# Performance work log

Hardware: AMD Instinct MI355X
Metric: run time of the kernel (lower is better)

The kernel has to match this reference:

```python
import jax, jax.numpy as jnp
import numpy as np

NUM_HEADS = 8
TOP_K = 2
ROUTER_EPS = 1e-5
LN_EPS = 1e-5
ROPE_BASE = 10000.0


def _layernorm(x, g, b):
    m = x.mean(-1, keepdims=True)
    v = ((x - m) ** 2).mean(-1, keepdims=True)
    return (x - m) * jax.lax.rsqrt(v + LN_EPS) * g + b


def _rope_tables(frames, height, width, head_dim, dtype):
    # dim split per axis; head_dim divisible by 3 with even parts (96 -> 32/32/32)
    dpa = head_dim // 3

    def freqs(n, d):
        inv = 1.0 / (ROPE_BASE ** (jnp.arange(0, d, 2, dtype=jnp.float32) / d))
        f = jnp.outer(jnp.arange(n, dtype=jnp.float32), inv)
        return jnp.concatenate([f, f], axis=-1)  # [n, d]

    fx, fy, ft = freqs(width, dpa), freqs(height, dpa), freqs(frames, dpa)

    def grid(ax, ay, at):
        gx = jnp.broadcast_to(ax[None, None, :, :], (frames, height, width, dpa))
        gy = jnp.broadcast_to(ay[None, :, None, :], (frames, height, width, dpa))
        gt = jnp.broadcast_to(at[:, None, None, :], (frames, height, width, dpa))
        return jnp.concatenate([gx, gy, gt], -1).reshape(frames * height * width, 3 * dpa)

    cos = grid(jnp.cos(fx), jnp.cos(fy), jnp.cos(ft)).astype(dtype)
    sin = grid(jnp.sin(fx), jnp.sin(fy), jnp.sin(ft)).astype(dtype)
    return cos, sin


def _apply_rope(x, cos, sin):
    # x: [B, H, S, hd]; cos/sin: [S, hd] (broadcast over B, H)
    h = x.shape[-1] // 2
    rot = jnp.concatenate([-x[..., h:], x[..., :h]], axis=-1)
    return x * cos + rot * sin


def _expert(x, g, u, d):
    # SwiGLU expert: down(silu(gate(x)) * up(x))
    return (jax.nn.silu(x @ g) * (x @ u)) @ d


def _block(x, cos, sin, ln1_g, ln1_b, w_qkv, w_out, gate_w,
           eg, eu, ed, sg, su, sd, ln2_g, ln2_b):
    B, S, D = x.shape
    hd = D // NUM_HEADS
    # --- 3D-RoPE attention (pre-LN, non-causal) ---
    xn = _layernorm(x, ln1_g, ln1_b)
    qkv = (xn @ w_qkv).reshape(B, S, 3, NUM_HEADS, hd)
    q = jnp.moveaxis(qkv[:, :, 0], 1, 2)  # [B, H, S, hd]
    k = jnp.moveaxis(qkv[:, :, 1], 1, 2)
    v = jnp.moveaxis(qkv[:, :, 2], 1, 2)
    q = _apply_rope(q, cos, sin)
    k = _apply_rope(k, cos, sin)
    scores = jnp.einsum('bhqd,bhkd->bhqk', q, k) * (hd ** -0.5)
    attn = jax.nn.softmax(scores, axis=-1)
    o = jnp.einsum('bhqk,bhkd->bhqd', attn, v)
    o = jnp.moveaxis(o, 1, 2).reshape(B, S, D) @ w_out
    x = x + o
    # --- temporal MoE (top-k routing + shared expert) ---
    xf = x.reshape(-1, D)
    probs = jax.nn.softmax(xf @ gate_w, axis=-1)
    topv, topi = jax.lax.top_k(probs, TOP_K)
    topv = topv / (topv.sum(-1, keepdims=True) + ROUTER_EPS)
    E = eg.shape[0]
    # combine weight per (token, expert): sum over k slots routed to that expert
    comb = jnp.sum(topv[..., None] * (topi[..., None] == jnp.arange(E)), axis=1)  # [N, E]
    out = _expert(xf, sg, su, sd)  # shared expert on all tokens
    for e in range(E):
        out = out + comb[:, e:e + 1] * _expert(xf, eg[e], eu[e], ed[e])
    return _layernorm(x + out.reshape(B, S, D), ln2_g, ln2_b)


def setup_inputs() -> dict:
    key = jax.random.key(0)
    ks = jax.random.split(key, 10)
    B, S, D, F, E, L = 2, 2048, 768, 3072, 4, 2
    s = 0.02
    return {
        'x': jax.random.normal(ks[0], (B, S, D), jnp.float32),
        'height': 16, 'width': 16, 'frames': 8,
        'ln1_g': jnp.ones((L, D), jnp.float32),
        'ln1_b': jnp.zeros((L, D), jnp.float32),
        'w_qkv': jax.random.normal(ks[1], (L, D, 3 * D), jnp.float32) * s,
        'w_out': jax.random.normal(ks[2], (L, D, D), jnp.float32) * s,
        'gate_w': jax.random.normal(ks[3], (L, D, E), jnp.float32) * 0.01,
        'eg': jax.random.normal(ks[4], (L, E, D, F), jnp.float32) * s,
        'eu': jax.random.normal(ks[5], (L, E, D, F), jnp.float32) * s,
        'ed': jax.random.normal(ks[6], (L, E, F, D), jnp.float32) * s,
        'sg': jax.random.normal(ks[7], (L, D, F), jnp.float32) * s,
        'su': jax.random.normal(ks[8], (L, D, F), jnp.float32) * s,
        'sd': jax.random.normal(ks[9], (L, F, D), jnp.float32) * s,
        'ln2_g': jnp.ones((L, D), jnp.float32),
        'ln2_b': jnp.zeros((L, D), jnp.float32),
    }


def reference(x, height, width, frames, ln1_g, ln1_b, w_qkv, w_out, gate_w,
              eg, eu, ed, sg, su, sd, ln2_g, ln2_b):
    hd = x.shape[-1] // NUM_HEADS
    cos, sin = _rope_tables(frames, height, width, hd, x.dtype)
    for i in range(ln1_g.shape[0]):
        x = _block(x, cos, sin, ln1_g[i], ln1_b[i], w_qkv[i], w_out[i], gate_w[i],
                   eg[i], eu[i], ed[i], sg[i], su[i], sd[i], ln2_g[i], ln2_b[i])
    return x
```

## Files before the change

### kernel.cpp

```cpp
#include <hip/hip_runtime.h>
#include <stdint.h>

#define S_LEN 2048
#define DM    768
#define NHEAD 8
#define HDIM  96
#define HDP   128
#define FF    3072
#define FF2   6144
#define NEXP  4
#define NTOK  4096
#define NBH   16
#define HBROWS (2 * NTOK)

typedef unsigned short u16;
typedef short bf16x8 __attribute__((ext_vector_type(8)));
typedef float f32x4 __attribute__((ext_vector_type(4)));
typedef __attribute__((address_space(1))) void* gptr_t;
typedef __attribute__((address_space(3))) void* lptr_t;

__device__ __forceinline__ u16 f2bf(float f) {
  union { float f; uint32_t u; } v; v.f = f;
  uint32_t r = v.u + 0x7FFFu + ((v.u >> 16) & 1u);
  return (u16)(r >> 16);
}
__device__ __forceinline__ float bf2f(u16 h) {
  union { uint32_t u; float f; } v; v.u = ((uint32_t)h) << 16;
  return v.f;
}
__device__ __forceinline__ void split2(float f, u16& hi, u16& lo) {
  u16 h = f2bf(f);
  lo = f2bf(f - bf2f(h));
  hi = h;
}
__device__ __forceinline__ float siluf(float g) {
  return g / (1.0f + expf(-g));
}
__device__ __forceinline__ void gload16(const void* g, void* l) {
  __builtin_amdgcn_global_load_lds((gptr_t)(void*)g, (lptr_t)l, 16, 0, 0);
}
__device__ __forceinline__ int swz(int byte) {
  return byte ^ (((byte >> 7) & 3) << 4);
}

template<int MODE>
__global__ __launch_bounds__(256) void gemm_nt(
    const u16* __restrict__ A, const u16* __restrict__ B, void* __restrict__ Cv,
    int M, int N, int K, int lda, int ldb, long sA, long sB, long sC, int kspl,
    u16* __restrict__ hb)
{
  __shared__ u16 As[2][128 * 32];
  __shared__ u16 Bs[2][128 * 32];
  const int z = blockIdx.z;
  const int bh = z / kspl;
  const int kc = z - bh * kspl;
  const u16* Az = A + (long)bh * sA;
  const u16* Bz = B + (long)bh * sB;
  const int brow = blockIdx.y << 7;
  const int bcol = blockIdx.x << 7;
  const int tid = threadIdx.x;
  const int wid = tid >> 6;
  const int lane = tid & 63;
  const int wr = (wid >> 1) << 6;
  const int wc = (wid & 1) << 6;

  f32x4 acc[4][4] = {};
  const int a0 = (wid << 11) + (lane << 4);

  auto stage = [&](int buf, int k0) {
#pragma unroll
    for (int c = 0; c < 2; ++c) {
      int ab = a0 + (c << 10);
      int lb = swz(ab);
      int row = ab >> 6;
      int kcol = (lb & 63) >> 1;
      int ld = (wid << 11) + (c << 10);
      gload16(Az + (long)(brow + row) * lda + (k0 + kcol), (char*)As[buf] + ld);
      gload16(Bz + (long)(bcol + row) * ldb + (k0 + kcol), (char*)Bs[buf] + ld);
    }
  };

  const int kt = K / kspl;
  const int kbeg = kc * kt;
  const int nt = kt >> 5;
  stage(0, kbeg);
  __syncthreads();
  for (int t = 0; t < nt; ++t) {
    const int cur = t & 1;
    if (t + 1 < nt) stage(cur ^ 1, kbeg + ((t + 1) << 5));
    bf16x8 af[4], bfr[4];
    const int lr = lane & 15;
    const int lk = (lane >> 4) << 4;
#pragma unroll
    for (int m = 0; m < 4; ++m)
      af[m] = *(const bf16x8*)((const char*)As[cur] + swz((((wr + m * 16 + lr) << 6) + lk)));
#pragma unroll
    for (int n = 0; n < 4; ++n)
      bfr[n] = *(const bf16x8*)((const char*)Bs[cur] + swz((((wc + n * 16 + lr) << 6) + lk)));
#pragma unroll
    for (int m = 0; m < 4; ++m)
#pragma unroll
      for (int n = 0; n < 4; ++n)
        acc[m][n] = __builtin_amdgcn_mfma_f32_16x16x32_bf16(af[m], bfr[n], acc[m][n], 0, 0, 0);
    if (t + 1 < nt) __syncthreads();
  }

  const int crow0 = brow + wr + ((lane >> 4) << 2);
  const int ccol0 = bcol + wc + (lane & 15);
  const long cbase = (long)bh * sC;
  if constexpr (MODE == 5) {
    const int pbase = (bcol + wc) >> 5;
#pragma unroll
    for (int m = 0; m < 4; ++m)
#pragma unroll
      for (int np = 0; np < 2; ++np)
#pragma unroll
        for (int j = 0; j < 4; ++j) {
          int r = crow0 + m * 16 + j;
          float g = acc[m][2 * np][j], u = acc[m][2 * np + 1][j];
          int hcol = ((pbase + np) << 4) + (lane & 15);
          hb[(long)r * FF + hcol] = f2bf(siluf(g) * u);
        }
  } else {
#pragma unroll
    for (int m = 0; m < 4; ++m)
#pragma unroll
      for (int n = 0; n < 4; ++n)
#pragma unroll
        for (int j = 0; j < 4; ++j) {
          long idx = cbase + (long)(crow0 + m * 16 + j) * N + (ccol0 + n * 16);
          float v = acc[m][n][j];
          if constexpr (MODE == 2) ((u16*)Cv)[idx] = f2bf(v);
          else if constexpr (MODE == 3) unsafeAtomicAdd((float*)Cv + idx, v);
          else ((float*)Cv)[idx] = v;
        }
  }
}

template<int MODE>
__global__ __launch_bounds__(256) void gemm3_nt(
    const u16* __restrict__ Ah, const u16* __restrict__ Al,
    const u16* __restrict__ Bh, const u16* __restrict__ Bl,
    float* __restrict__ C,
    int M, int N, int K, int lda, int ldb, long sA, long sB, long sC, int kspl,
    u16* __restrict__ hbh, u16* __restrict__ hbl)
{
  __shared__ u16 Ash[2][128 * 32], Asl[2][128 * 32];
  __shared__ u16 Bsh[2][128 * 32], Bsl[2][128 * 32];
  const int z = blockIdx.z;
  const int bh = z / kspl;
  const int kc = z - bh * kspl;
  const u16* Azh = Ah + (long)bh * sA;
  const u16* Azl = Al + (long)bh * sA;
  const u16* Bzh = Bh + (long)bh * sB;
  const u16* Bzl = Bl + (long)bh * sB;
  const int brow = blockIdx.y << 7;
  const int bcol = blockIdx.x << 7;
  const int tid = threadIdx.x;
  const int wid = tid >> 6;
  const int lane = tid & 63;
  const int wr = (wid >> 1) << 6;
  const int wc = (wid & 1) << 6;

  f32x4 acc[4][4] = {};
  const int a0 = (wid << 11) + (lane << 4);

  auto stage = [&](int buf, int k0) {
#pragma unroll
    for (int c = 0; c < 2; ++c) {
      int ab = a0 + (c << 10);
      int lb = swz(ab);
      int row = ab >> 6;
      int kcol = (lb & 63) >> 1;
      long ao = (long)(brow + row) * lda + (k0 + kcol);
      long bo = (long)(bcol + row) * ldb + (k0 + kcol);
      int ld = (wid << 11) + (c << 10);
      gload16(Azh + ao, (char*)Ash[buf] + ld);
      gload16(Azl + ao, (char*)Asl[buf] + ld);
      gload16(Bzh + bo, (char*)Bsh[buf] + ld);
      gload16(Bzl + bo, (char*)Bsl[buf] + ld);
    }
  };

  const int kt = K / kspl;
  const int kbeg = kc * kt;
  const int nt = kt >> 5;
  stage(0, kbeg);
  __syncthreads();
  for (int t = 0; t < nt; ++t) {
    const int cur = t & 1;
    if (t + 1 < nt) stage(cur ^ 1, kbeg + ((t + 1) << 5));
    const int lr = lane & 15;
    const int lk = (lane >> 4) << 4;
    bf16x8 ah[4], al[4], bh_[4], bl[4];
#pragma unroll
    for (int m = 0; m < 4; ++m) {
      int off = swz(((wr + m * 16 + lr) << 6) + lk);
      ah[m] = *(const bf16x8*)((const char*)Ash[cur] + off);
      al[m] = *(const bf16x8*)((const char*)Asl[cur] + off);
    }
#pragma unroll
    for (int n = 0; n < 4; ++n) {
      int off = swz(((wc + n * 16 + lr) << 6) + lk);
      bh_[n] = *(const bf16x8*)((const char*)Bsh[cur] + off);
      bl[n] = *(const bf16x8*)((const char*)Bsl[cur] + off);
    }
#pragma unroll
    for (int m = 0; m < 4; ++m)
#pragma unroll
      for (int n = 0; n < 4; ++n) {
        acc[m][n] = __builtin_amdgcn_mfma_f32_16x16x32_bf16(al[m], bh_[n], acc[m][n], 0, 0, 0);
        acc[m][n] = __builtin_amdgcn_mfma_f32_16x16x32_bf16(ah[m], bl[n], acc[m][n], 0, 0, 0);
        acc[m][n] = __builtin_amdgcn_mfma_f32_16x16x32_bf16(ah[m], bh_[n], acc[m][n], 0, 0, 0);
      }
    if (t + 1 < nt) __syncthreads();
  }

  const int crow0 = brow + wr + ((lane >> 4) << 2);
  const int ccol0 = bcol + wc + (lane & 15);
  const long cbase = (long)bh * sC;
  if constexpr (MODE == 5) {
    const int pbase = (bcol + wc) >> 5;
#pragma unroll
    for (int m = 0; m < 4; ++m)
#pragma unroll
      for (int np = 0; np < 2; ++np)
#pragma unroll
        for (int j = 0; j < 4; ++j) {
          int r = crow0 + m * 16 + j;
          float g = acc[m][2 * np][j], u = acc[m][2 * np + 1][j];
          float h = siluf(g) * u;
          int hcol = ((pbase + np) << 4) + (lane & 15);
          u16 hh, ll; split2(h, hh, ll);
          hbh[(long)r * FF + hcol] = hh;
          hbl[(long)r * FF + hcol] = ll;
        }
  } else {
#pragma unroll
    for (int m = 0; m < 4; ++m)
#pragma unroll
      for (int n = 0; n < 4; ++n)
#pragma unroll
        for (int j = 0; j < 4; ++j) {
          long idx = cbase + (long)(crow0 + m * 16 + j) * N + (ccol0 + n * 16);
          if constexpr (MODE == 3) unsafeAtomicAdd(&C[idx], acc[m][n][j]);
          else C[idx] = acc[m][n][j];
        }
  }
}

template<int MODE>
__global__ __launch_bounds__(256) void gemm3i_nt(
    const u16* __restrict__ Ah, const u16* __restrict__ Al,
    const u16* __restrict__ Bh, const u16* __restrict__ Bl,
    float* __restrict__ C, int N, int K, int lda, int ldb, int ldc,
    const int* __restrict__ perm, const int* __restrict__ cnt,
    const int* __restrict__ cbase, int kspl, long wstride,
    u16* __restrict__ hbh, u16* __restrict__ hbl, const float* __restrict__ comb)
{
  const int z = blockIdx.z;
  const int e = z / kspl;
  const int kc = z - e * kspl;
  const int cn = cnt[e];
  const int brow = blockIdx.y << 7;
  if (brow >= cn) return;
  const int cb = cbase[e];
  const int* pe = perm + e * NTOK;
  const u16* Bhe = Bh + (long)e * wstride;
  const u16* Ble = Bl + (long)e * wstride;
  __shared__ u16 Ash[2][128 * 32], Asl[2][128 * 32];
  __shared__ u16 Bsh[2][128 * 32], Bsl[2][128 * 32];
  const int bcol = blockIdx.x << 7;
  const int tid = threadIdx.x;
  const int wid = tid >> 6;
  const int lane = tid & 63;
  const int wr = (wid >> 1) << 6;
  const int wc = (wid & 1) << 6;

  f32x4 acc[4][4] = {};
  const int a0 = (wid << 11) + (lane << 4);

  int arow[2];
#pragma unroll
  for (int c = 0; c < 2; ++c) {
    int ab = a0 + (c << 10);
    int row = ab >> 6;
    int g = brow + row;
    if constexpr (MODE == 5) {
      arow[c] = (g < cn) ? pe[g] : pe[brow];
    } else {
      arow[c] = cb + ((g < cn) ? g : (cn - 1));
    }
  }

  auto stage = [&](int buf, int k0) {
#pragma unroll
    for (int c = 0; c < 2; ++c) {
      int ab = a0 + (c << 10);
      int lb = swz(ab);
      int row = ab >> 6;
      int kcol = (lb & 63) >> 1;
      int ld = (wid << 11) + (c << 10);
      gload16(Ah + (long)arow[c] * lda + (k0 + kcol), (char*)Ash[buf] + ld);
      gload16(Al + (long)arow[c] * lda + (k0 + kcol), (char*)Asl[buf] + ld);
      long bo = (long)(bcol + row) * ldb + (k0 + kcol);
      gload16(Bhe + bo, (char*)Bsh[buf] + ld);
      gload16(Ble + bo, (char*)Bsl[buf] + ld);
    }
  };

  const int kt = K / kspl;
  const int kbeg = kc * kt;
  const int nt = kt >> 5;
  stage(0, kbeg);
  __syncthreads();
  for (int t = 0; t < nt; ++t) {
    const int cur = t & 1;
    if (t + 1 < nt) stage(cur ^ 1, kbeg + ((t + 1) << 5));
    const int lr = lane & 15;
    const int lk = (lane >> 4) << 4;
    bf16x8 ah[4], al[4], bh_[4], bl[4];
#pragma unroll
    for (int m = 0; m < 4; ++m) {
      int off = swz(((wr + m * 16 + lr) << 6) + lk);
      ah[m] = *(const bf16x8*)((const char*)Ash[cur] + off);
      al[m] = *(const bf16x8*)((const char*)Asl[cur] + off);
    }
#pragma unroll
    for (int n = 0; n < 4; ++n) {
      int off = swz(((wc + n * 16 + lr) << 6) + lk);
      bh_[n] = *(const bf16x8*)((const char*)Bsh[cur] + off);
      bl[n] = *(const bf16x8*)((const char*)Bsl[cur] + off);
    }
#pragma unroll
    for (int m = 0; m < 4; ++m)
#pragma unroll
      for (int n = 0; n < 4; ++n) {
        acc[m][n] = __builtin_amdgcn_mfma_f32_16x16x32_bf16(al[m], bh_[n], acc[m][n], 0, 0, 0);
        acc[m][n] = __builtin_amdgcn_mfma_f32_16x16x32_bf16(ah[m], bl[n], acc[m][n], 0, 0, 0);
        acc[m][n] = __builtin_amdgcn_mfma_f32_16x16x32_bf16(ah[m], bh_[n], acc[m][n], 0, 0, 0);
      }
    if (t + 1 < nt) __syncthreads();
  }

  const int crow0 = brow + wr + ((lane >> 4) << 2);
  const int ccol0 = bcol + wc + (lane & 15);
  if constexpr (MODE == 5) {
    const int pbase = (bcol + wc) >> 5;
#pragma unroll
    for (int m = 0; m < 4; ++m)
#pragma unroll
      for (int j = 0; j < 4; ++j) {
        int r = crow0 + m * 16 + j;
        if (r < cn) {
          float w = comb[pe[r] * 4 + e];
#pragma unroll
          for (int np = 0; np < 2; ++np) {
            float g = acc[m][2 * np][j], u = acc[m][2 * np + 1][j];
            float h = siluf(g) * u * w;
            int hcol = ((pbase + np) << 4) + (lane & 15);
            u16 hh, ll; split2(h, hh, ll);
            hbh[(long)(cb + r) * FF + hcol] = hh;
            hbl[(long)(cb + r) * FF + hcol] = ll;
          }
        }
      }
  } else {
#pragma unroll
    for (int m = 0; m < 4; ++m)
#pragma unroll
      for (int n = 0; n < 4; ++n)
#pragma unroll
        for (int j = 0; j < 4; ++j) {
          int r = crow0 + m * 16 + j;
          if (r < cn) {
            int col = ccol0 + n * 16;
            unsafeAtomicAdd(&C[(long)pe[r] * ldc + col], acc[m][n][j]);
          }
        }
  }
}

template<int MODE>
__global__ __launch_bounds__(256) void gemmi_nt(
    const u16* __restrict__ A, const u16* __restrict__ B, void* __restrict__ Cv,
    int N, int K, int lda, int ldb, int ldc,
    const int* __restrict__ perm, const int* __restrict__ cnt,
    const int* __restrict__ cbase, int kspl, long wstride,
    u16* __restrict__ hb, const float* __restrict__ comb)
{
  const int z = blockIdx.z;
  const int e = z / kspl;
  const int kc = z - e * kspl;
  const int cn = cnt[e];
  const int brow = blockIdx.y << 7;
  if (brow >= cn) return;
  const int cb = cbase[e];
  const int* pe = perm + e * NTOK;
  const u16* Be = B + (long)e * wstride;
  __shared__ u16 As[2][128 * 32];
  __shared__ u16 Bs[2][128 * 32];
  const int bcol = blockIdx.x << 7;
  const int tid = threadIdx.x;
  const int wid = tid >> 6;
  const int lane = tid & 63;
  const int wr = (wid >> 1) << 6;
  const int wc = (wid & 1) << 6;

  f32x4 acc[4][4] = {};
  const int a0 = (wid << 11) + (lane << 4);

  int arow[2];
#pragma unroll
  for (int c = 0; c < 2; ++c) {
    int ab = a0 + (c << 10);
    int row = ab >> 6;
    int g = brow + row;
    if constexpr (MODE == 5) {
      arow[c] = (g < cn) ? pe[g] : pe[brow];
    } else {
      arow[c] = cb + ((g < cn) ? g : (cn - 1));
    }
  }

  auto stage = [&](int buf, int k0) {
#pragma unroll
    for (int c = 0; c < 2; ++c) {
      int ab = a0 + (c << 10);
      int lb = swz(ab);
      int row = ab >> 6;
      int kcol = (lb & 63) >> 1;
      int ld = (wid << 11) + (c << 10);
      gload16(A + (long)arow[c] * lda + (k0 + kcol), (char*)As[buf] + ld);
      gload16(Be + (long)(bcol + row) * ldb + (k0 + kcol), (char*)Bs[buf] + ld);
    }
  };

  const int kt = K / kspl;
  const int kbeg = kc * kt;
  const int nt = kt >> 5;
  stage(0, kbeg);
  __syncthreads();
  for (int t = 0; t < nt; ++t) {
    const int cur = t & 1;
    if (t + 1 < nt) stage(cur ^ 1, kbeg + ((t + 1) << 5));
    bf16x8 af[4], bfr[4];
    const int lr = lane & 15;
    const int lk = (lane >> 4) << 4;
#pragma unroll
    for (int m = 0; m < 4; ++m)
      af[m] = *(const bf16x8*)((const char*)As[cur] + swz((((wr + m * 16 + lr) << 6) + lk)));
#pragma unroll
    for (int n = 0; n < 4; ++n)
      bfr[n] = *(const bf16x8*)((const char*)Bs[cur] + swz((((wc + n * 16 + lr) << 6) + lk)));
#pragma unroll
    for (int m = 0; m < 4; ++m)
#pragma unroll
      for (int n = 0; n < 4; ++n)
        acc[m][n] = __builtin_amdgcn_mfma_f32_16x16x32_bf16(af[m], bfr[n], acc[m][n], 0, 0, 0);
    if (t + 1 < nt) __syncthreads();
  }

  const int crow0 = brow + wr + ((lane >> 4) << 2);
  const int ccol0 = bcol + wc + (lane & 15);
  if constexpr (MODE == 5) {
    const int pbase = (bcol + wc) >> 5;
#pragma unroll
    for (int m = 0; m < 4; ++m)
#pragma unroll
      for (int j = 0; j < 4; ++j) {
        int r = crow0 + m * 16 + j;
        if (r < cn) {
          float w = comb[pe[r] * 4 + e];
#pragma unroll
          for (int np = 0; np < 2; ++np) {
            float g = acc[m][2 * np][j], u = acc[m][2 * np + 1][j];
            int hcol = ((pbase + np) << 4) + (lane & 15);
            hb[(long)(cb + r) * FF + hcol] = f2bf(siluf(g) * u * w);
          }
        }
      }
  } else {
#pragma unroll
    for (int m = 0; m < 4; ++m)
#pragma unroll
      for (int n = 0; n < 4; ++n)
#pragma unroll
        for (int j = 0; j < 4; ++j) {
          int r = crow0 + m * 16 + j;
          if (r < cn) {
            int col = ccol0 + n * 16;
            unsafeAtomicAdd((float*)Cv + (long)pe[r] * ldc + col, acc[m][n][j]);
          }
        }
  }
}

__global__ __launch_bounds__(256, 2) void fattn_k(
    const u16* __restrict__ qh, const u16* __restrict__ ql,
    const u16* __restrict__ kh, const u16* __restrict__ kl,
    const u16* __restrict__ vth, const u16* __restrict__ vtl,
    u16* __restrict__ omh, u16* __restrict__ oml, float scale)
{
  __shared__ u16 Ksh[64 * 128], Ksl[64 * 128];
  __shared__ u16 Vsh[128 * 64], Vsl[128 * 64];
  const int bh = blockIdx.x;
  const int qt = blockIdx.y;
  const int tid = threadIdx.x, wid = tid >> 6, lane = tid & 63;
  const int lr = lane & 15, lg = lane >> 4;
  const int q0 = qt * 64 + wid * 16;
  const long bhoff = (long)bh * S_LEN * HDP;
  const u16* Qh = qh + bhoff;  const u16* Ql = ql + bhoff;
  const u16* Kgh = kh + bhoff; const u16* Kgl = kl + bhoff;
  const u16* Vgh = vth + bhoff; const u16* Vgl = vtl + bhoff;

  bf16x8 qfh[4], qfl[4];
#pragma unroll
  for (int kk = 0; kk < 4; ++kk) {
    long o = (long)(q0 + lr) * HDP + kk * 32 + lg * 8;
    qfh[kk] = *(const bf16x8*)(Qh + o);
    qfl[kk] = *(const bf16x8*)(Ql + o);
  }

  f32x4 oacc[6] = {};
  float rm[4], rls[4];
#pragma unroll
  for (int j = 0; j < 4; ++j) { rm[j] = -1e30f; rls[j] = 0.f; }

  for (int t = 0; t < S_LEN / 64; ++t) {
    __syncthreads();
#pragma unroll
    for (int c = 0; c < 4; ++c) {
      int off = (tid + (c << 8)) << 4;
      {
        int lb = off ^ ((((off >> 8) & 7)) << 4);
        int row = lb >> 8, colh = (lb & 255) >> 1;
        long src = (long)(t * 64 + row) * HDP + colh;
        gload16(Kgh + src, (char*)Ksh + off);
        gload16(Kgl + src, (char*)Ksl + off);
      }
      {
        int lb = off ^ ((((off >> 7) & 7)) << 4);
        int row = lb >> 7, colh = (lb & 127) >> 1;
        long src = (long)row * S_LEN + t * 64 + colh;
        gload16(Vgh + src, (char*)Vsh + off);
        gload16(Vgl + src, (char*)Vsl + off);
      }
    }
    __syncthreads();

    f32x4 sacc[4] = {};
#pragma unroll
    for (int kk = 0; kk < 4; ++kk) {
      bf16x8 kbh[4], kbl[4];
#pragma unroll
      for (int n = 0; n < 4; ++n) {
        int byte = ((n * 16 + lr) << 8) + (kk << 6) + (lg << 4);
        byte ^= ((byte >> 8) & 7) << 4;
        kbh[n] = *(const bf16x8*)((const char*)Ksh + byte);
        kbl[n] = *(const bf16x8*)((const char*)Ksl + byte);
      }
      __builtin_amdgcn_s_setprio(1);
#pragma unroll
      for (int n = 0; n < 4; ++n) {
        sacc[n] = __builtin_amdgcn_mfma_f32_16x16x32_bf16(qfl[kk], kbh[n], sacc[n], 0, 0, 0);
        sacc[n] = __builtin_amdgcn_mfma_f32_16x16x32_bf16(qfh[kk], kbl[n], sacc[n], 0, 0, 0);
        sacc[n] = __builtin_amdgcn_mfma_f32_16x16x32_bf16(qfh[kk], kbh[n], sacc[n], 0, 0, 0);
      }
      __builtin_amdgcn_s_setprio(0);
    }
    __syncthreads();

#pragma unroll
    for (int j = 0; j < 4; ++j) {
      float mx = fmaxf(fmaxf(sacc[0][j], sacc[1][j]),
                       fmaxf(sacc[2][j], sacc[3][j])) * scale;
      mx = fmaxf(mx, __shfl_xor(mx, 1));
      mx = fmaxf(mx, __shfl_xor(mx, 2));
      mx = fmaxf(mx, __shfl_xor(mx, 4));
      mx = fmaxf(mx, __shfl_xor(mx, 8));
      float mnew = fmaxf(rm[j], mx);
      float corr = __expf(rm[j] - mnew);
      rm[j] = mnew;
      float ps = 0.f;
#pragma unroll
      for (int n = 0; n < 4; ++n) {
        float p = __expf(sacc[n][j] * scale - mnew);
        sacc[n][j] = p; ps += p;
      }
      ps += __shfl_xor(ps, 1); ps += __shfl_xor(ps, 2);
      ps += __shfl_xor(ps, 4); ps += __shfl_xor(ps, 8);
      rls[j] = rls[j] * corr + ps;
#pragma unroll
      for (int n2 = 0; n2 < 6; ++n2) oacc[n2][j] *= corr;
    }

    char* Pwh = (char*)Ksh + (wid << 11);
    char* Pwl = (char*)Ksl + (wid << 11);
#pragma unroll
    for (int n = 0; n < 4; ++n)
#pragma unroll
      for (int j = 0; j < 4; ++j) {
        int row = lg * 4 + j;
        int byte = (row << 7) + ((n * 16 + lr) << 1);
        byte ^= ((byte >> 7) & 7) << 4;
        u16 h, l; split2(sacc[n][j], h, l);
        *(u16*)(Pwh + byte) = h;
        *(u16*)(Pwl + byte) = l;
      }
    bf16x8 pah[2], pal[2];
#pragma unroll
    for (int kk = 0; kk < 2; ++kk) {
      int byte = (lr << 7) + (kk << 6) + (lg << 4);
      byte ^= ((byte >> 7) & 7) << 4;
      pah[kk] = *(const bf16x8*)(Pwh + byte);
      pal[kk] = *(const bf16x8*)(Pwl + byte);
    }

#pragma unroll
    for (int kk = 0; kk < 2; ++kk) {
      bf16x8 vbh[6], vbl[6];
#pragma unroll
      for (int n2 = 0; n2 < 6; ++n2) {
        int byte = ((n2 * 16 + lr) << 7) + (kk << 6) + (lg << 4);
        byte ^= ((byte >> 7) & 7) << 4;
        vbh[n2] = *(const bf16x8*)((const char*)Vsh + byte);
        vbl[n2] = *(const bf16x8*)((const char*)Vsl + byte);
      }
      __builtin_amdgcn_s_setprio(1);
#pragma unroll
      for (int n2 = 0; n2 < 6; ++n2) {
        oacc[n2] = __builtin_amdgcn_mfma_f32_16x16x32_bf16(pal[kk], vbh[n2], oacc[n2], 0, 0, 0);
        oacc[n2] = __builtin_amdgcn_mfma_f32_16x16x32_bf16(pah[kk], vbl[n2], oacc[n2], 0, 0, 0);
        oacc[n2] = __builtin_amdgcn_mfma_f32_16x16x32_bf16(pah[kk], vbh[n2], oacc[n2], 0, 0, 0);
      }
      __builtin_amdgcn_s_setprio(0);
    }
  }

  const int b = bh >> 3, h = bh & 7;
#pragma unroll
  for (int j = 0; j < 4; ++j) {
    float inv = 1.0f / rls[j];
    int q = q0 + lg * 4 + j;
    long base = ((long)(b * S_LEN + q)) * DM + h * HDIM;
#pragma unroll
    for (int n2 = 0; n2 < 6; ++n2) {
      int d = n2 * 16 + lr;
      u16 hh, ll; split2(oacc[n2][j] * inv, hh, ll);
      omh[base + d] = hh; oml[base + d] = ll;
    }
  }
}

__global__ void wconv_t(const float* __restrict__ in, u16* __restrict__ outh,
                        u16* __restrict__ outl, int R, int C, int ilv,
                        long inStride, long outStride) {
  __shared__ float tile[32][33];
  long z = blockIdx.z;
  in += z * inStride; outh += z * outStride;
  if (outl) outl += z * outStride;
  int c0 = blockIdx.x << 5, r0 = blockIdx.y << 5;
  int tx = threadIdx.x;
  for (int rr = threadIdx.y; rr < 32; rr += 8)
    tile[rr][tx] = in[(long)(r0 + rr) * C + (c0 + tx)];
  __syncthreads();
  for (int rr = threadIdx.y; rr < 32; rr += 8) {
    u16 h, l; split2(tile[tx][rr], h, l);
    int f = c0 + rr;
    long orow = (ilv < 0) ? f : (((f >> 4) << 5) + (ilv << 4) + (f & 15));
    long o = orow * R + (r0 + tx);
    outh[o] = h;
    if (outl) outl[o] = l;
  }
}

__global__ __launch_bounds__(256) void ln_k(const float* __restrict__ in,
    const float* __restrict__ g, const float* __restrict__ b,
    float* __restrict__ outf, u16* __restrict__ outh, u16* __restrict__ outl) {
  int row = blockIdx.x;
  const float* x = in + (long)row * DM;
  int tid = threadIdx.x;
  float v[3], s = 0.f, ss = 0.f;
#pragma unroll
  for (int i = 0; i < 3; ++i) { v[i] = x[tid + (i << 8)]; s += v[i]; ss += v[i] * v[i]; }
  __shared__ float red[2][4];
  for (int o = 32; o; o >>= 1) { s += __shfl_down(s, o); ss += __shfl_down(ss, o); }
  int wid = tid >> 6, lane = tid & 63;
  if (!lane) { red[0][wid] = s; red[1][wid] = ss; }
  __syncthreads();
  s = red[0][0] + red[0][1] + red[0][2] + red[0][3];
  ss = red[1][0] + red[1][1] + red[1][2] + red[1][3];
  float mean = s * (1.f / DM);
  float var = ss * (1.f / DM) - mean * mean;
  float rs = rsqrtf(var + 1e-5f);
#pragma unroll
  for (int i = 0; i < 3; ++i) {
    int c = tid + (i << 8);
    float y = (v[i] - mean) * rs * g[c] + b[c];
    if (outf) outf[(long)row * DM + c] = y;
    if (outh) { u16 h, l; split2(y, h, l); outh[(long)row * DM + c] = h; outl[(long)row * DM + c] = l; }
  }
}

__global__ void rope_tables_k(float* __restrict__ cosT, float* __restrict__ sinT) {
  int s = blockIdx.x, d = threadIdx.x;
  int xc = s & 15, y = (s >> 4) & 15, t = s >> 8;
  int axis = d / 32, fi = d & 15;
  int coord = axis == 0 ? xc : (axis == 1 ? y : t);
  float inv = powf(10000.0f, -(float)fi / 16.0f);
  float ang = (float)coord * inv;
  cosT[s * HDIM + d] = cosf(ang);
  sinT[s * HDIM + d] = sinf(ang);
}

__global__ __launch_bounds__(256) void rope_apply_k(const float* __restrict__ qkv,
    const float* __restrict__ cosT, const float* __restrict__ sinT,
    u16* __restrict__ qh, u16* __restrict__ ql,
    u16* __restrict__ kh, u16* __restrict__ kl) {
  int bs = blockIdx.x;
  int b = bs >> 11, s = bs & 2047;
  const float* base = qkv + ((long)(b * S_LEN + s) * 3) * DM;
  for (int idx = threadIdx.x; idx < DM; idx += 256) {
    int h = idx / HDIM, d = idx - h * HDIM;
    float c = cosT[s * HDIM + d], sn = sinT[s * HDIM + d];
    int pair = (d < 48) ? idx + 48 : idx - 48;
    float qv = base[idx], kv = base[DM + idx];
    float qr = (d < 48) ? -base[pair] : base[pair];
    float kr = (d < 48) ? -base[DM + pair] : base[DM + pair];
    long o = ((long)(b * NHEAD + h) * S_LEN + s) * HDP + d;
    u16 hh, ll;
    split2(qv * c + qr * sn, hh, ll); qh[o] = hh; ql[o] = ll;
    split2(kv * c + kr * sn, hh, ll); kh[o] = hh; kl[o] = ll;
  }
  int t = threadIdx.x;
  int h = t >> 5, d = HDIM + (t & 31);
  long o = ((long)(b * NHEAD + h) * S_LEN + s) * HDP + d;
  qh[o] = 0; ql[o] = 0; kh[o] = 0; kl[o] = 0;
}

__global__ void v_transpose_k(const float* __restrict__ qkv,
                              u16* __restrict__ vh, u16* __restrict__ vl) {
  __shared__ float tile[32][33];
  int bh = blockIdx.z, b = bh >> 3, h = bh & 7;
  int s0 = blockIdx.x << 5, d0 = blockIdx.y << 5;
  int tx = threadIdx.x;
  for (int r = threadIdx.y; r < 32; r += 8) {
    int s = s0 + r, d = d0 + tx;
    float v = 0.f;
    if (d < HDIM) v = qkv[((long)(b * S_LEN + s) * 3 + 2) * DM + h * HDIM + d];
    tile[r][tx] = v;
  }
  __syncthreads();
  for (int r = threadIdx.y; r < 32; r += 8) {
    int d = d0 + r;
    u16 hh, ll; split2(tile[tx][r], hh, ll);
    long o = ((long)bh * HDP + d) * S_LEN + (s0 + tx);
    vh[o] = hh; vl[o] = ll;
  }
}

__global__ __launch_bounds__(256) void router_k(const float* __restrict__ x,
    const float* __restrict__ gw, float* __restrict__ comb, int* __restrict__ mask) {
  int tok = blockIdx.x * 4 + (threadIdx.x >> 6);
  int lane = threadIdx.x & 63;
  const float* xr = x + (long)tok * DM;
  float a0 = 0, a1 = 0, a2 = 0, a3 = 0;
  for (int i = lane; i < DM; i += 64) {
    float xv = xr[i];
    const float* g = gw + i * 4;
    a0 += xv * g[0]; a1 += xv * g[1]; a2 += xv * g[2]; a3 += xv * g[3];
  }
  for (int o = 32; o; o >>= 1) {
    a0 += __shfl_down(a0, o); a1 += __shfl_down(a1, o);
    a2 += __shfl_down(a2, o); a3 += __shfl_down(a3, o);
  }
  if (lane == 0) {
    float p[4] = {a0, a1, a2, a3};
    float mx = fmaxf(fmaxf(p[0], p[1]), fmaxf(p[2], p[3]));
    float s = 0.f;
    for (int e = 0; e < 4; ++e) { p[e] = expf(p[e] - mx); s += p[e]; }
    for (int e = 0; e < 4; ++e) p[e] /= s;
    int i1 = 0;
    for (int e = 1; e < 4; ++e) if (p[e] > p[i1]) i1 = e;
    int i2 = -1;
    for (int e = 0; e < 4; ++e) if (e != i1 && (i2 < 0 || p[e] > p[i2])) i2 = e;
    float ssum = p[i1] + p[i2] + 1e-5f;
    float out[4] = {0, 0, 0, 0};
    out[i1] = p[i1] / ssum; out[i2] = p[i2] / ssum;
    for (int e = 0; e < 4; ++e) comb[tok * 4 + e] = out[e];
    mask[tok] = (1 << i1) | (1 << i2);
  }
}

__global__ void scan_k(const int* __restrict__ mask, int* __restrict__ perm,
                       int* __restrict__ cnt) {
  __shared__ int sd[256];
  __shared__ int base;
  int tid = threadIdx.x;
  int e = blockIdx.x;
  if (tid == 0) base = 0;
  __syncthreads();
  for (int c = 0; c < NTOK / 256; ++c) {
    int tok = c * 256 + tid;
    int f = (mask[tok] >> e) & 1;
    sd[tid] = f;
    __syncthreads();
    for (int s = 1; s < 256; s <<= 1) {
      int v = (tid >= s) ? sd[tid - s] : 0;
      __syncthreads();
      sd[tid] += v;
      __syncthreads();
    }
    if (f) perm[e * NTOK + base + sd[tid] - 1] = tok;
    int tot = sd[255];
    __syncthreads();
    if (tid == 0) base += tot;
    __syncthreads();
  }
  if (tid == 0) cnt[e] = base;
}

__global__ void cbase_k(const int* __restrict__ cnt, int* __restrict__ cbase) {
  if (threadIdx.x == 0) {
    int b = 0;
    for (int e = 0; e < NEXP; ++e) { cbase[e] = b; b += cnt[e]; }
  }
}

__global__ void f2b_k(const float* __restrict__ src, u16* __restrict__ dst, long n) {
  long i = (long)blockIdx.x * 256 + threadIdx.x;
  if (i < n) dst[i] = f2bf(src[i]);
}

__global__ void f2bsplit_k(const float* __restrict__ src, u16* __restrict__ dh,
                           u16* __restrict__ dl, long n) {
  long i = (long)blockIdx.x * 256 + threadIdx.x;
  if (i < n) { u16 h, l; split2(src[i], h, l); dh[i] = h; dl[i] = l; }
}

extern "C" void kernel_launch(void* const* d_in, const int* in_sizes, int n_in,
                              void* d_out, int out_size, void* d_ws, size_t ws_size,
                              hipStream_t stream) {
  (void)in_sizes; (void)n_in; (void)out_size; (void)ws_size;
  const float* x_in  = (const float*)d_in[0];
  const float* ln1_g = (const float*)d_in[4];
  const float* ln1_b = (const float*)d_in[5];
  const float* w_qkv = (const float*)d_in[6];
  const float* w_out = (const float*)d_in[7];
  const float* gatew = (const float*)d_in[8];
  const float* eg    = (const float*)d_in[9];
  const float* eu    = (const float*)d_in[10];
  const float* ed    = (const float*)d_in[11];
  const float* sg    = (const float*)d_in[12];
  const float* su    = (const float*)d_in[13];
  const float* sd    = (const float*)d_in[14];
  const float* ln2_g = (const float*)d_in[15];
  const float* ln2_b = (const float*)d_in[16];

  float* xc = (float*)d_out;
  char* W = (char*)d_ws;
  size_t off = 0;
  auto alloc = [&](size_t bytes) {
    size_t o = off; off = (off + bytes + 255) & ~(size_t)255; return o;
  };
  size_t o_cos  = alloc((size_t)S_LEN * HDIM * 4);
  size_t o_sin  = alloc((size_t)S_LEN * HDIM * 4);
  size_t o_xnh  = alloc((size_t)NTOK * DM * 2);
  size_t o_xnl  = alloc((size_t)NTOK * DM * 2);
  size_t o_comb = alloc((size_t)NTOK * 4 * 4);
  size_t o_mask = alloc((size_t)NTOK * 4);
  size_t o_perm = alloc((size_t)NEXP * NTOK * 4);
  size_t o_cnt  = alloc(256);
  size_t o_cb   = alloc(256);
  const size_t EGU_B = (size_t)NEXP * FF2 * DM * 2;
  const size_t SGU_B = (size_t)FF2 * DM * 2;
  const size_t SD_B  = (size_t)DM * FF * 2;
  const size_t A_BYTES = 2 * EGU_B + 2 * SGU_B + 2 * SD_B;
  size_t oA = alloc(A_BYTES);
  size_t o_qkv = oA;
  size_t o_qph = oA + (size_t)NTOK * 3 * DM * 4;
  size_t o_qpl = o_qph + (size_t)NBH * S_LEN * HDP * 2;
  size_t o_kph = o_qpl + (size_t)NBH * S_LEN * HDP * 2;
  size_t o_kpl = o_kph + (size_t)NBH * S_LEN * HDP * 2;
  size_t o_vth = o_kpl + (size_t)NBH * S_LEN * HDP * 2;
  size_t o_vtl = o_vth + (size_t)NBH * HDP * S_LEN * 2;
  size_t o_omh = o_vtl + (size_t)NBH * HDP * S_LEN * 2;
  size_t o_oml = o_omh + (size_t)NTOK * DM * 2;
  size_t o_eguh = oA;
  size_t o_egul = oA + EGU_B;
  size_t o_sguh = oA + 2 * EGU_B;
  size_t o_sgul = o_sguh + SGU_B;
  size_t o_sdh  = o_sgul + SGU_B;
  size_t o_sdl  = o_sdh + SD_B;
  size_t o_edh  = oA;
  size_t o_edl  = oA + (size_t)NEXP * DM * FF * 2;
  const size_t H_BYTES = (size_t)2 * HBROWS * FF * 2;
  size_t oH = alloc(H_BYTES);
  size_t o_wqh = oH;
  size_t o_wql = o_wqh + (size_t)3 * DM * DM * 2;
  size_t o_woh = o_wql + (size_t)3 * DM * DM * 2;
  size_t o_wol = o_woh + (size_t)DM * DM * 2;
  size_t o_hbh = oH;
  size_t o_hbl = oH + (size_t)HBROWS * FF * 2;

  float* cosT = (float*)(W + o_cos);
  float* sinT = (float*)(W + o_sin);
  u16*   xnh  = (u16*)(W + o_xnh);
  u16*   xnl  = (u16*)(W + o_xnl);
  float* comb = (float*)(W + o_comb);
  int* maskb  = (int*)(W + o_mask);
  int* permb  = (int*)(W + o_perm);
  int* cntb   = (int*)(W + o_cnt);
  int* cbaseb = (int*)(W + o_cb);
  float* qkv  = (float*)(W + o_qkv);
  u16 *qph = (u16*)(W + o_qph), *qpl = (u16*)(W + o_qpl);
  u16 *kph = (u16*)(W + o_kph), *kpl = (u16*)(W + o_kpl);
  u16 *vth = (u16*)(W + o_vth), *vtl = (u16*)(W + o_vtl);
  u16 *omh = (u16*)(W + o_omh), *oml = (u16*)(W + o_oml);
  u16 *eguh = (u16*)(W + o_eguh), *egul = (u16*)(W + o_egul);
  u16 *sguh = (u16*)(W + o_sguh), *sgul = (u16*)(W + o_sgul);
  u16 *sdh = (u16*)(W + o_sdh), *sdl = (u16*)(W + o_sdl);
  u16 *edh = (u16*)(W + o_edh), *edl = (u16*)(W + o_edl);
  u16 *wqh = (u16*)(W + o_wqh), *wql = (u16*)(W + o_wql);
  u16 *woh = (u16*)(W + o_woh), *wol = (u16*)(W + o_wol);
  u16 *hbh = (u16*)(W + o_hbh), *hbl = (u16*)(W + o_hbl);

  const long ND = (long)NTOK * DM;
  const int gND = (int)((ND + 255) / 256);

  hipMemcpyAsync(xc, x_in, (size_t)ND * 4, hipMemcpyDeviceToDevice, stream);
  rope_tables_k<<<S_LEN, HDIM, 0, stream>>>(cosT, sinT);

  dim3 tb(32, 8, 1);
  for (int l = 0; l < 2; ++l) {
    const float* wqkv_l = w_qkv + (size_t)l * DM * 3 * DM;
    const float* wout_l = w_out + (size_t)l * DM * DM;
    const float* gw_l   = gatew + (size_t)l * DM * 4;
    const float* eg_l = eg + (size_t)l * NEXP * DM * FF;
    const float* eu_l = eu + (size_t)l * NEXP * DM * FF;
    const float* ed_l = ed + (size_t)l * NEXP * FF * DM;
    const float* sg_l = sg + (size_t)l * DM * FF;
    const float* su_l = su + (size_t)l * DM * FF;
    const float* sd_l = sd + (size_t)l * FF * DM;

    wconv_t<<<dim3(3 * DM / 32, DM / 32, 1), tb, 0, stream>>>(wqkv_l, wqh, wql, DM, 3 * DM, -1, 0, 0);
    wconv_t<<<dim3(DM / 32, DM / 32, 1), tb, 0, stream>>>(wout_l, woh, wol, DM, DM, -1, 0, 0);

    ln_k<<<NTOK, 256, 0, stream>>>(xc, ln1_g + l * DM, ln1_b + l * DM, nullptr, xnh, xnl);
    gemm3_nt<0><<<dim3(3 * DM >> 7, NTOK >> 7, 1), 256, 0, stream>>>(
        xnh, xnl, wqh, wql, qkv, NTOK, 3 * DM, DM, DM, DM, 0, 0, 0, 1, nullptr, nullptr);
    rope_apply_k<<<NTOK, 256, 0, stream>>>(qkv, cosT, sinT, qph, qpl, kph, kpl);
    v_transpose_k<<<dim3(S_LEN / 32, HDP / 32, NBH), tb, 0, stream>>>(qkv, vth, vtl);
    fattn_k<<<dim3(NBH, S_LEN / 64), dim3(256), 0, stream>>>(
        qph, qpl, kph, kpl, vth, vtl, omh, oml, 0.10206207261596575f);
    gemm3_nt<3><<<dim3(DM >> 7, NTOK >> 7, 2), 256, 0, stream>>>(
        omh, oml, woh, wol, xc, NTOK, DM, DM, DM, DM, 0, 0, 0, 2, nullptr, nullptr);

    router_k<<<NTOK / 4, 256, 0, stream>>>(xc, gw_l, comb, maskb);
    scan_k<<<NEXP, 256, 0, stream>>>(maskb, permb, cntb);
    cbase_k<<<1, 64, 0, stream>>>(cntb, cbaseb);

    if (l == 0) {
      wconv_t<<<dim3(FF / 32, DM / 32, 1), tb, 0, stream>>>(sg_l, sguh, sgul, DM, FF, 0, 0, 0);
      wconv_t<<<dim3(FF / 32, DM / 32, 1), tb, 0, stream>>>(su_l, sguh, sgul, DM, FF, 1, 0, 0);
      wconv_t<<<dim3(DM / 32, FF / 32, 1), tb, 0, stream>>>(sd_l, sdh, sdl, FF, DM, -1, 0, 0);
      wconv_t<<<dim3(FF / 32, DM / 32, NEXP), tb, 0, stream>>>(
          eg_l, eguh, egul, DM, FF, 0, (long)DM * FF, (long)FF2 * DM);
      wconv_t<<<dim3(FF / 32, DM / 32, NEXP), tb, 0, stream>>>(
          eu_l, eguh, egul, DM, FF, 1, (long)DM * FF, (long)FF2 * DM);

      f2bsplit_k<<<gND, 256, 0, stream>>>(xc, xnh, xnl, ND);
      gemm3_nt<5><<<dim3(FF2 >> 7, NTOK >> 7, 1), 256, 0, stream>>>(
          xnh, xnl, sguh, sgul, nullptr, NTOK, FF2, DM, DM, DM, 0, 0, 0, 1, hbh, hbl);
      gemm3_nt<3><<<dim3(DM >> 7, NTOK >> 7, 4), 256, 0, stream>>>(
          hbh, hbl, sdh, sdl, xc, NTOK, DM, FF, FF, FF, 0, 0, 0, 4, nullptr, nullptr);
      gemm3i_nt<5><<<dim3(FF2 >> 7, NTOK >> 7, NEXP), 256, 0, stream>>>(
          xnh, xnl, eguh, egul, nullptr, FF2, DM, DM, DM, FF2,
          permb, cntb, cbaseb, 1, (long)FF2 * DM, hbh, hbl, comb);
      wconv_t<<<dim3(DM / 32, FF / 32, NEXP), tb, 0, stream>>>(
          ed_l, edh, edl, FF, DM, -1, (long)FF * DM, (long)DM * FF);
      gemm3i_nt<1><<<dim3(DM >> 7, NTOK >> 7, NEXP * 2), 256, 0, stream>>>(
          hbh, hbl, edh, edl, xc, DM, FF, FF, FF, DM,
          permb, cntb, cbaseb, 2, (long)DM * FF, nullptr, nullptr, nullptr);
    } else {
      wconv_t<<<dim3(FF / 32, DM / 32, 1), tb, 0, stream>>>(sg_l, sguh, nullptr, DM, FF, 0, 0, 0);
      wconv_t<<<dim3(FF / 32, DM / 32, 1), tb, 0, stream>>>(su_l, sguh, nullptr, DM, FF, 1, 0, 0);
      wconv_t<<<dim3(DM / 32, FF / 32, 1), tb, 0, stream>>>(sd_l, sdh, nullptr, FF, DM, -1, 0, 0);
      wconv_t<<<dim3(FF / 32, DM / 32, NEXP), tb, 0, stream>>>(
          eg_l, eguh, nullptr, DM, FF, 0, (long)DM * FF, (long)FF2 * DM);
      wconv_t<<<dim3(FF / 32, DM / 32, NEXP), tb, 0, stream>>>(
          eu_l, eguh, nullptr, DM, FF, 1, (long)DM * FF, (long)FF2 * DM);

      f2b_k<<<gND, 256, 0, stream>>>(xc, xnh, ND);
      gemm_nt<5><<<dim3(FF2 >> 7, NTOK >> 7, 1), 256, 0, stream>>>(
          xnh, sguh, nullptr, NTOK, FF2, DM, DM, DM, 0, 0, 0, 1, hbh);
      gemm_nt<3><<<dim3(DM >> 7, NTOK >> 7, 4), 256, 0, stream>>>(
          hbh, sdh, xc, NTOK, DM, FF, FF, FF, 0, 0, 0, 4, nullptr);
      gemmi_nt<5><<<dim3(FF2 >> 7, NTOK >> 7, NEXP), 256, 0, stream>>>(
          xnh, eguh, nullptr, FF2, DM, DM, DM, FF2,
          permb, cntb, cbaseb, 1, (long)FF2 * DM, hbh, comb);
      wconv_t<<<dim3(DM / 32, FF / 32, NEXP), tb, 0, stream>>>(
          ed_l, edh, nullptr, FF, DM, -1, (long)FF * DM, (long)DM * FF);
      gemmi_nt<3><<<dim3(DM >> 7, NTOK >> 7, NEXP * 2), 256, 0, stream>>>(
          hbh, edh, xc, DM, FF, FF, FF, DM,
          permb, cntb, cbaseb, 2, (long)DM * FF, nullptr, nullptr);
    }
    ln_k<<<NTOK, 256, 0, stream>>>(xc, ln2_g + l * DM, ln2_b + l * DM, xc, nullptr, nullptr);
  }
}
```

Before: 1.850 ms.

## Swap GEMM grid axes, skip padded head-dim in attention, raise expert-down split-K

```diff
diff --git a/kernel.cpp b/kernel.cpp
--- a/kernel.cpp
+++ b/kernel.cpp
@@ -56,8 +56,8 @@
   const int kc = z - bh * kspl;
   const u16* Az = A + (long)bh * sA;
   const u16* Bz = B + (long)bh * sB;
-  const int brow = blockIdx.y << 7;
-  const int bcol = blockIdx.x << 7;
+  const int brow = blockIdx.x << 7;
+  const int bcol = blockIdx.y << 7;
   const int tid = threadIdx.x;
   const int wid = tid >> 6;
   const int lane = tid & 63;
@@ -154,8 +154,8 @@
   const u16* Azl = Al + (long)bh * sA;
   const u16* Bzh = Bh + (long)bh * sB;
   const u16* Bzl = Bl + (long)bh * sB;
-  const int brow = blockIdx.y << 7;
-  const int bcol = blockIdx.x << 7;
+  const int brow = blockIdx.x << 7;
+  const int bcol = blockIdx.y << 7;
   const int tid = threadIdx.x;
   const int wid = tid >> 6;
   const int lane = tid & 63;
@@ -262,7 +262,7 @@
   const int e = z / kspl;
   const int kc = z - e * kspl;
   const int cn = cnt[e];
-  const int brow = blockIdx.y << 7;
+  const int brow = blockIdx.x << 7;
   if (brow >= cn) return;
   const int cb = cbase[e];
   const int* pe = perm + e * NTOK;
@@ -270,7 +270,7 @@
   const u16* Ble = Bl + (long)e * wstride;
   __shared__ u16 Ash[2][128 * 32], Asl[2][128 * 32];
   __shared__ u16 Bsh[2][128 * 32], Bsl[2][128 * 32];
-  const int bcol = blockIdx.x << 7;
+  const int bcol = blockIdx.y << 7;
   const int tid = threadIdx.x;
   const int wid = tid >> 6;
   const int lane = tid & 63;
@@ -393,14 +393,14 @@
   const int e = z / kspl;
   const int kc = z - e * kspl;
   const int cn = cnt[e];
-  const int brow = blockIdx.y << 7;
+  const int brow = blockIdx.x << 7;
   if (brow >= cn) return;
   const int cb = cbase[e];
   const int* pe = perm + e * NTOK;
   const u16* Be = B + (long)e * wstride;
   __shared__ u16 As[2][128 * 32];
   __shared__ u16 Bs[2][128 * 32];
-  const int bcol = blockIdx.x << 7;
+  const int bcol = blockIdx.y << 7;
   const int tid = threadIdx.x;
   const int wid = tid >> 6;
   const int lane = tid & 63;
@@ -514,9 +514,9 @@
   const u16* Kgh = kh + bhoff; const u16* Kgl = kl + bhoff;
   const u16* Vgh = vth + bhoff; const u16* Vgl = vtl + bhoff;
 
-  bf16x8 qfh[4], qfl[4];
-#pragma unroll
-  for (int kk = 0; kk < 4; ++kk) {
+  bf16x8 qfh[3], qfl[3];
+#pragma unroll
+  for (int kk = 0; kk < 3; ++kk) {
     long o = (long)(q0 + lr) * HDP + kk * 32 + lg * 8;
     qfh[kk] = *(const bf16x8*)(Qh + o);
     qfl[kk] = *(const bf16x8*)(Ql + o);
@@ -551,7 +551,7 @@
 
     f32x4 sacc[4] = {};
 #pragma unroll
-    for (int kk = 0; kk < 4; ++kk) {
+    for (int kk = 0; kk < 3; ++kk) {
       bf16x8 kbh[4], kbl[4];
 #pragma unroll
       for (int n = 0; n < 4; ++n) {
@@ -948,13 +948,13 @@
     wconv_t<<<dim3(DM / 32, DM / 32, 1), tb, 0, stream>>>(wout_l, woh, wol, DM, DM, -1, 0, 0);
 
     ln_k<<<NTOK, 256, 0, stream>>>(xc, ln1_g + l * DM, ln1_b + l * DM, nullptr, xnh, xnl);
-    gemm3_nt<0><<<dim3(3 * DM >> 7, NTOK >> 7, 1), 256, 0, stream>>>(
+    gemm3_nt<0><<<dim3(NTOK >> 7, 3 * DM >> 7, 1), 256, 0, stream>>>(
         xnh, xnl, wqh, wql, qkv, NTOK, 3 * DM, DM, DM, DM, 0, 0, 0, 1, nullptr, nullptr);
     rope_apply_k<<<NTOK, 256, 0, stream>>>(qkv, cosT, sinT, qph, qpl, kph, kpl);
     v_transpose_k<<<dim3(S_LEN / 32, HDP / 32, NBH), tb, 0, stream>>>(qkv, vth, vtl);
     fattn_k<<<dim3(NBH, S_LEN / 64), dim3(256), 0, stream>>>(
         qph, qpl, kph, kpl, vth, vtl, omh, oml, 0.10206207261596575f);
-    gemm3_nt<3><<<dim3(DM >> 7, NTOK >> 7, 2), 256, 0, stream>>>(
+    gemm3_nt<3><<<dim3(NTOK >> 7, DM >> 7, 2), 256, 0, stream>>>(
         omh, oml, woh, wol, xc, NTOK, DM, DM, DM, DM, 0, 0, 0, 2, nullptr, nullptr);
 
     router_k<<<NTOK / 4, 256, 0, stream>>>(xc, gw_l, comb, maskb);
@@ -971,18 +971,18 @@
           eu_l, eguh, egul, DM, FF, 1, (long)DM * FF, (long)FF2 * DM);
 
       f2bsplit_k<<<gND, 256, 0, stream>>>(xc, xnh, xnl, ND);
-      gemm3_nt<5><<<dim3(FF2 >> 7, NTOK >> 7, 1), 256, 0, stream>>>(
+      gemm3_nt<5><<<dim3(NTOK >> 7, FF2 >> 7, 1), 256, 0, stream>>>(
           xnh, xnl, sguh, sgul, nullptr, NTOK, FF2, DM, DM, DM, 0, 0, 0, 1, hbh, hbl);
-      gemm3_nt<3><<<dim3(DM >> 7, NTOK >> 7, 4), 256, 0, stream>>>(
+      gemm3_nt<3><<<dim3(NTOK >> 7, DM >> 7, 4), 256, 0, stream>>>(
           hbh, hbl, sdh, sdl, xc, NTOK, DM, FF, FF, FF, 0, 0, 0, 4, nullptr, nullptr);
-      gemm3i_nt<5><<<dim3(FF2 >> 7, NTOK >> 7, NEXP), 256, 0, stream>>>(
+      gemm3i_nt<5><<<dim3(NTOK >> 7, FF2 >> 7, NEXP), 256, 0, stream>>>(
           xnh, xnl, eguh, egul, nullptr, FF2, DM, DM, DM, FF2,
           permb, cntb, cbaseb, 1, (long)FF2 * DM, hbh, hbl, comb);
       wconv_t<<<dim3(DM / 32, FF / 32, NEXP), tb, 0, stream>>>(
           ed_l, edh, edl, FF, DM, -1, (long)FF * DM, (long)DM * FF);
-      gemm3i_nt<1><<<dim3(DM >> 7, NTOK >> 7, NEXP * 2), 256, 0, stream>>>(
+      gemm3i_nt<1><<<dim3(NTOK >> 7, DM >> 7, NEXP * 4), 256, 0, stream>>>(
           hbh, hbl, edh, edl, xc, DM, FF, FF, FF, DM,
-          permb, cntb, cbaseb, 2, (long)DM * FF, nullptr, nullptr, nullptr);
+          permb, cntb, cbaseb, 4, (long)DM * FF, nullptr, nullptr, nullptr);
     } else {
       wconv_t<<<dim3(FF / 32, DM / 32, 1), tb, 0, stream>>>(sg_l, sguh, nullptr, DM, FF, 0, 0, 0);
       wconv_t<<<dim3(FF / 32, DM / 32, 1), tb, 0, stream>>>(su_l, sguh, nullptr, DM, FF, 1, 0, 0);
@@ -993,18 +993,18 @@
           eu_l, eguh, nullptr, DM, FF, 1, (long)DM * FF, (long)FF2 * DM);
 
       f2b_k<<<gND, 256, 0, stream>>>(xc, xnh, ND);
-      gemm_nt<5><<<dim3(FF2 >> 7, NTOK >> 7, 1), 256, 0, stream>>>(
+      gemm_nt<5><<<dim3(NTOK >> 7, FF2 >> 7, 1), 256, 0, stream>>>(
           xnh, sguh, nullptr, NTOK, FF2, DM, DM, DM, 0, 0, 0, 1, hbh);
-      gemm_nt<3><<<dim3(DM >> 7, NTOK >> 7, 4), 256, 0, stream>>>(
+      gemm_nt<3><<<dim3(NTOK >> 7, DM >> 7, 4), 256, 0, stream>>>(
           hbh, sdh, xc, NTOK, DM, FF, FF, FF, 0, 0, 0, 4, nullptr);
-      gemmi_nt<5><<<dim3(FF2 >> 7, NTOK >> 7, NEXP), 256, 0, stream>>>(
+      gemmi_nt<5><<<dim3(NTOK >> 7, FF2 >> 7, NEXP), 256, 0, stream>>>(
           xnh, eguh, nullptr, FF2, DM, DM, DM, FF2,
           permb, cntb, cbaseb, 1, (long)FF2 * DM, hbh, comb);
       wconv_t<<<dim3(DM / 32, FF / 32, NEXP), tb, 0, stream>>>(
           ed_l, edh, nullptr, FF, DM, -1, (long)FF * DM, (long)DM * FF);
-      gemmi_nt<3><<<dim3(DM >> 7, NTOK >> 7, NEXP * 2), 256, 0, stream>>>(
+      gemmi_nt<3><<<dim3(NTOK >> 7, DM >> 7, NEXP * 4), 256, 0, stream>>>(
           hbh, edh, xc, DM, FF, FF, FF, DM,
-          permb, cntb, cbaseb, 2, (long)DM * FF, nullptr, nullptr);
+          permb, cntb, cbaseb, 4, (long)DM * FF, nullptr, nullptr);
     }
     ln_k<<<NTOK, 256, 0, stream>>>(xc, ln2_g + l * DM, ln2_b + l * DM, xc, nullptr, nullptr);
   }
```

Result: slower. 2.260 ms (+22.2%).
